# Optimization experiments

Measured on AMD Instinct MI355X. Metric: run time of the kernel, lower is better.

The kernel has to match this reference:

```python
import jax, jax.numpy as jnp
import numpy as np

EMBED_DIM = 1024
NUM_HEADS = 16
HEAD_DIM = EMBED_DIM // NUM_HEADS
L = 1024  # target/source seq len
N = 2     # batch
EPS = 1e-6


def setup_inputs() -> dict:
    key = jax.random.key(0)
    ks = jax.random.split(key, 11)
    s = 0.02
    return {
        "query": jax.random.normal(ks[0], (L, N, EMBED_DIM), jnp.float32),
        "key": jax.random.normal(ks[1], (L, N, EMBED_DIM), jnp.float32),
        "value": jax.random.normal(ks[2], (L, N, EMBED_DIM), jnp.float32),
        "Wq": jax.random.normal(ks[3], (EMBED_DIM, EMBED_DIM), jnp.float32) * s,
        "bq": jnp.zeros((EMBED_DIM,), jnp.float32),
        "Wk": jax.random.normal(ks[4], (EMBED_DIM, EMBED_DIM), jnp.float32) * s,
        "bk": jnp.zeros((EMBED_DIM,), jnp.float32),
        "Wv": jax.random.normal(ks[5], (EMBED_DIM, EMBED_DIM), jnp.float32) * s,
        "bv": jnp.zeros((EMBED_DIM,), jnp.float32),
        "Wo": jax.random.normal(ks[6], (EMBED_DIM, EMBED_DIM), jnp.float32) * s,
        "bo": jnp.zeros((EMBED_DIM,), jnp.float32),
    }


def _feature_map(x):
    # phi(x) = elu(x) + 1 (Katharopoulos et al., 2020)
    return jax.nn.elu(x) + 1.0


def reference(query, key, value, Wq, bq, Wk, bk, Wv, bv, Wo, bo):
    tgt_len, bsz, embed_dim = query.shape
    H, d = NUM_HEADS, HEAD_DIM
    # projections (torch Linear: x @ W.T + b)
    q = query @ Wq.T + bq
    k = key @ Wk.T + bk
    v = value @ Wv.T + bv
    # (L, N, E) -> (N*H, L, d)
    def to_heads(x):
        return x.reshape(-1, bsz * H, d).transpose(1, 0, 2)
    q, k, v = to_heads(q), to_heads(k), to_heads(v)
    q = _feature_map(q)
    k = _feature_map(k)
    # causal linear attention: S_t = cumsum_s<=t k_s v_s^T ; z_t = cumsum k_s
    kv = jnp.cumsum(jnp.einsum('bld,ble->blde', k, v), axis=1)  # (B*H, L, d, d)
    num = jnp.einsum('bld,blde->ble', q, kv)                    # (B*H, L, d)
    z = jnp.cumsum(k, axis=1)                                   # (B*H, L, d)
    denom = jnp.einsum('bld,bld->bl', q, z) + EPS               # (B*H, L)
    attn = num / denom[..., None]
    # (N*H, L, d) -> (L, N, E)
    attn = attn.transpose(1, 0, 2).reshape(tgt_len, bsz, embed_dim)
    return attn @ Wo.T + bo
```

## Files before the change

### kernel.cpp

```cpp
#include <hip/hip_runtime.h>
#include <cmath>


#define EPS 1e-6f

typedef short bf16x8 __attribute__((ext_vector_type(8)));
typedef float f32x4 __attribute__((ext_vector_type(4)));

__device__ __forceinline__ float b2f(ushort u) {
    union { unsigned u32; float f; } x; x.u32 = ((unsigned)u) << 16; return x.f;
}
__device__ __forceinline__ ushort f2b(float f) {
    union { float f; unsigned u; } x; x.f = f;
    unsigned r = (x.u + 0x7fffu + ((x.u >> 16) & 1u)) >> 16;
    return (ushort)r;
}
__device__ __forceinline__ void gload16(const void* g, void* l) {
    __builtin_amdgcn_global_load_lds(
        (__attribute__((address_space(1))) void*)(uintptr_t)g,
        (__attribute__((address_space(3))) void*)l,
        16, 0, 0);
}

template<int KSTEPS>
__device__ __forceinline__ void gemm_mainloop8(const ushort* __restrict__ A,
                                               const ushort* __restrict__ B,
                                               int brow, int bcol, int kbeg,
                                               ushort* Sh, f32x4 acc[4][4]) {
    const int K = 1024;
    const int BUFE = 8192;
    int tid = threadIdx.x;
    int w = tid >> 6, lane = tid & 63;
    int fr = lane & 15, hi = lane >> 4;
    int wr = w >> 1, wc = w & 1;

    const ushort* gsrc[4];
    int ldst[4];
    #pragma unroll
    for (int i = 0; i < 4; i++) {
        int s = (w * 4 + i) * 64 + lane;
        const ushort* base; int r, c;
        if (s < 512) { r = s >> 2; c = s & 3; base = A + (size_t)(brow + r) * K; }
        else { int s2 = s - 512; r = s2 >> 2; c = s2 & 3; base = B + (size_t)(bcol + r) * K; }
        gsrc[i] = base + kbeg + ((c ^ ((r >> 1) & 3)) * 8);
        ldst[i] = (w * 4 + i) * 512;
    }

    int ea[4], eb[4];
    #pragma unroll
    for (int m = 0; m < 4; m++) {
        int ra = wr * 64 + m * 16 + fr;
        ea[m] = ra * 32 + ((hi ^ ((ra >> 1) & 3)) * 8);
    }
    #pragma unroll
    for (int n = 0; n < 4; n++) {
        int rb = wc * 64 + n * 16 + fr;
        eb[n] = 4096 + rb * 32 + ((hi ^ ((rb >> 1) & 3)) * 8);
    }

    #pragma unroll
    for (int m = 0; m < 4; m++)
        #pragma unroll
        for (int n = 0; n < 4; n++)
            acc[m][n] = (f32x4){0.f, 0.f, 0.f, 0.f};

    #pragma unroll
    for (int i = 0; i < 4; i++) gload16(gsrc[i], Sh + ldst[i]);
    __syncthreads();

    for (int t = 0; t < KSTEPS; ++t) {
        if (t + 1 < KSTEPS) {
            ushort* Sn = Sh + ((t + 1) & 1) * BUFE;
            #pragma unroll
            for (int i = 0; i < 4; i++) gload16(gsrc[i] + (t + 1) * 32, Sn + ldst[i]);
        }
        const ushort* Bc = Sh + (t & 1) * BUFE;
        bf16x8 af[4], bf[4];
        #pragma unroll
        for (int m = 0; m < 4; m++) af[m] = *(const bf16x8*)&Bc[ea[m]];
        #pragma unroll
        for (int n = 0; n < 4; n++) bf[n] = *(const bf16x8*)&Bc[eb[n]];
        #pragma unroll
        for (int m = 0; m < 4; m++)
            #pragma unroll
            for (int n = 0; n < 4; n++)
                acc[m][n] = __builtin_amdgcn_mfma_f32_16x16x32_bf16(af[m], bf[n], acc[m][n], 0, 0, 0);
        __syncthreads();
    }
}

__global__ __launch_bounds__(256) void gemm_proj(
    const ushort* __restrict__ Aq, const ushort* __restrict__ Ak, const ushort* __restrict__ Av,
    const ushort* __restrict__ Bq, const ushort* __restrict__ Bk, const ushort* __restrict__ Bv,
    ushort* __restrict__ pbuf) {
    __shared__ ushort Sh[2 * 8192];
    int bid = blockIdx.x;
    int swz = (bid & 7) * 96 + (bid >> 3);
    int z = swz >> 8;
    int rem = swz & 255;
    int kh = rem >> 7;
    int rem2 = rem & 127;
    int brow = (rem2 >> 3) * 128, bcol = (rem2 & 7) * 128;
    const ushort* A = (z == 0) ? Aq : (z == 1) ? Ak : Av;
    const ushort* B = (z == 0) ? Bq : (z == 1) ? Bk : Bv;
    f32x4 acc[4][4];
    gemm_mainloop8<16>(A, B, brow, bcol, kh * 512, Sh, acc);
    int tid = threadIdx.x, w = tid >> 6, lane = tid & 63;
    int fr = lane & 15, hi = lane >> 4;
    int wr = w >> 1, wc = w & 1;
    ushort* pp = pbuf + (size_t)(z * 2 + kh) * 2097152;
    #pragma unroll
    for (int m = 0; m < 4; m++)
        #pragma unroll
        for (int n = 0; n < 4; n++)
            #pragma unroll
            for (int r = 0; r < 4; r++) {
                int grow = brow + wr * 64 + m * 16 + hi * 4 + r;
                int gcol = bcol + wc * 64 + n * 16 + fr;
                pp[(size_t)grow * 1024 + gcol] = f2b(acc[m][n][r]);
            }
}

__global__ __launch_bounds__(256) void combine_proj(const ushort* __restrict__ pbuf,
                                                    const float* __restrict__ bq,
                                                    const float* __restrict__ bk,
                                                    const float* __restrict__ bv,
                                                    ushort* __restrict__ oq,
                                                    ushort* __restrict__ ok,
                                                    ushort* __restrict__ ov) {
    int z = blockIdx.z;
    int idx = blockIdx.x * 256 + threadIdx.x;
    int row = idx >> 7, c0 = (idx & 127) * 8;
    const float* bias = (z == 0) ? bq : (z == 1) ? bk : bv;
    const ushort* p0 = pbuf + (size_t)(z * 2) * 2097152 + (size_t)row * 1024 + c0;
    bf16x8 a = *(const bf16x8*)p0;
    bf16x8 b = *(const bf16x8*)(p0 + 2097152);
    int l = row >> 1, nb = row & 1, h = c0 >> 6, dd0 = c0 & 63;
    float v[8];
    #pragma unroll
    for (int j = 0; j < 8; j++)
        v[j] = b2f((ushort)a[j]) + b2f((ushort)b[j]) + bias[c0 + j];
    if (z < 2) {
        bf16x8 o;
        #pragma unroll
        for (int j = 0; j < 8; j++) {
            float t = (v[j] > 0.f) ? v[j] + 1.f : __expf(v[j]);
            o[j] = (short)f2b(t);
        }
        ushort* out = (z == 0) ? oq : ok;
        *(bf16x8*)&out[(size_t)((nb * 16 + h) * 1024 + l) * 64 + dd0] = o;
    } else {
        #pragma unroll
        for (int j = 0; j < 8; j++)
            ov[(size_t)((nb * 16 + h) * 64 + dd0 + j) * 1024 + l] = f2b(v[j]);
    }
}

__global__ __launch_bounds__(256) void gemm_outk(const ushort* __restrict__ A,
                                                 const ushort* __restrict__ B,
                                                 ushort* __restrict__ pbuf) {
    __shared__ ushort Sh[2 * 8192];
    int bid = blockIdx.x;
    int swz = (bid & 7) * 64 + (bid >> 3);
    int z = swz >> 7;
    int rem = swz & 127;
    int brow = (rem >> 3) * 128, bcol = (rem & 7) * 128;
    f32x4 acc[4][4];
    gemm_mainloop8<8>(A, B, brow, bcol, z * 256, Sh, acc);
    int tid = threadIdx.x, w = tid >> 6, lane = tid & 63;
    int fr = lane & 15, hi = lane >> 4;
    int wr = w >> 1, wc = w & 1;
    ushort* pp = pbuf + (size_t)z * 2097152;
    #pragma unroll
    for (int m = 0; m < 4; m++)
        #pragma unroll
        for (int n = 0; n < 4; n++)
            #pragma unroll
            for (int r = 0; r < 4; r++) {
                int grow = brow + wr * 64 + m * 16 + hi * 4 + r;
                int gcol = bcol + wc * 64 + n * 16 + fr;
                pp[(size_t)grow * 1024 + gcol] = f2b(acc[m][n][r]);
            }
}

__global__ __launch_bounds__(256) void reduce_out(const ushort* __restrict__ pbuf,
                                                  const float* __restrict__ bias,
                                                  float* __restrict__ out) {
    int idx = blockIdx.x * 256 + threadIdx.x;
    int row = idx >> 7, c0 = (idx & 127) * 8;
    const ushort* p = pbuf + (size_t)row * 1024 + c0;
    bf16x8 a = *(const bf16x8*)p;
    bf16x8 b = *(const bf16x8*)(p + 2097152);
    bf16x8 c = *(const bf16x8*)(p + 4194304);
    bf16x8 d = *(const bf16x8*)(p + 6291456);
    float* o = out + (size_t)row * 1024 + c0;
    #pragma unroll
    for (int j = 0; j < 8; j++)
        o[j] = b2f((ushort)a[j]) + b2f((ushort)b[j]) + b2f((ushort)c[j]) +
               b2f((ushort)d[j]) + bias[c0 + j];
}

__global__ __launch_bounds__(256) void cast_all(
    const float* __restrict__ i0, const float* __restrict__ i1, const float* __restrict__ i2,
    const float* __restrict__ i3, const float* __restrict__ i4, const float* __restrict__ i5,
    const float* __restrict__ i6,
    ushort* __restrict__ o0, ushort* __restrict__ o1, ushort* __restrict__ o2,
    ushort* __restrict__ o3, ushort* __restrict__ o4, ushort* __restrict__ o5,
    ushort* __restrict__ o6) {
    int z = blockIdx.z;
    const float* in = (z == 0) ? i0 : (z == 1) ? i1 : (z == 2) ? i2 :
                      (z == 3) ? i3 : (z == 4) ? i4 : (z == 5) ? i5 : i6;
    ushort* out = (z == 0) ? o0 : (z == 1) ? o1 : (z == 2) ? o2 :
                  (z == 3) ? o3 : (z == 4) ? o4 : (z == 5) ? o5 : o6;
    int n4 = (z < 3) ? 524288 : 262144;
    int i = blockIdx.x * 256 + threadIdx.x;
    if (i < n4) {
        float4 f = ((const float4*)in)[i];
        ushort4 o; o.x = f2b(f.x); o.y = f2b(f.y); o.z = f2b(f.z); o.w = f2b(f.w);
        ((ushort4*)out)[i] = o;
    }
}

__global__ __launch_bounds__(256) void chunk_sums(const ushort* __restrict__ kh,
                                                  const ushort* __restrict__ vt,
                                                  float* __restrict__ St,
                                                  float* __restrict__ zc) {
    int c = blockIdx.x, b = blockIdx.y, tid = threadIdx.x;
    __shared__ float Kl[64][64];
    __shared__ float Vl[64][65];
    const ushort* Kg = kh + (size_t)(b * 1024 + c * 64) * 64;
    for (int i = tid; i < 1024; i += 256) {
        ushort4 k4 = ((const ushort4*)Kg)[i];
        ((float4*)Kl)[i] = make_float4(b2f(k4.x), b2f(k4.y), b2f(k4.z), b2f(k4.w));
        int e = i >> 4, s4 = (i & 15) << 2;
        ushort4 v4 = *(const ushort4*)&vt[(size_t)(b * 64 + e) * 1024 + c * 64 + s4];
        Vl[e][s4 + 0] = b2f(v4.x); Vl[e][s4 + 1] = b2f(v4.y);
        Vl[e][s4 + 2] = b2f(v4.z); Vl[e][s4 + 3] = b2f(v4.w);
    }
    __syncthreads();
    int e = tid & 63, d0 = (tid >> 6) * 16;
    float s[16] = {};
    for (int ss = 0; ss < 64; ss++) {
        float ve = Vl[e][ss];
        #pragma unroll
        for (int i = 0; i < 16; i++) s[i] += Kl[ss][d0 + i] * ve;
    }
    float* So = St + (size_t)(b * 16 + c) * 4096 + e * 64 + d0;
    #pragma unroll
    for (int k = 0; k < 4; k++)
        *(float4*)&So[k * 4] = make_float4(s[4*k], s[4*k+1], s[4*k+2], s[4*k+3]);
    if (tid < 64) {
        float z = 0.f;
        for (int ss = 0; ss < 64; ss++) z += Kl[ss][tid];
        zc[(size_t)(b * 16 + c) * 64 + tid] = z;
    }
}

__global__ __launch_bounds__(256) void prefix_chunks(const float* __restrict__ St,
                                                     ushort* __restrict__ Spt,
                                                     float* __restrict__ zc) {
    int b = blockIdx.x, by = blockIdx.y, tid = threadIdx.x;
    int e = by * 16 + (tid >> 4);
    int d0 = (tid & 15) * 4;
    size_t base = (size_t)b * 65536 + (size_t)e * 64 + d0;
    float run[4] = {};
    for (int c = 0; c < 16; c++) {
        float4 v = *(const float4*)&St[base + (size_t)c * 4096];
        ushort4 o;
        o.x = f2b(run[0]); o.y = f2b(run[1]); o.z = f2b(run[2]); o.w = f2b(run[3]);
        *(ushort4*)&Spt[base + (size_t)c * 4096] = o;
        run[0] += v.x; run[1] += v.y; run[2] += v.z; run[3] += v.w;
    }
    if (by == 0 && tid < 64) {
        float rz = 0.f;
        for (int c = 0; c < 16; c++) {
            size_t idx = ((size_t)b * 16 + c) * 64 + tid;
            float t = zc[idx];
            zc[idx] = rz;
            rz += t;
        }
    }
}

__global__ __launch_bounds__(256) void attn_chunk(const ushort* __restrict__ qh,
                                                  const ushort* __restrict__ kh,
                                                  const ushort* __restrict__ vt,
                                                  const ushort* __restrict__ Spt,
                                                  const float* __restrict__ zc,
                                                  ushort* __restrict__ attn) {
    int c = blockIdx.x, b = blockIdx.y, tid = threadIdx.x;
    int w = tid >> 6, lane = tid & 63;
    int fr = lane & 15, hi = lane >> 4;
    __shared__ ushort Q[4096], Kt[4096], VT[4096], SP[4096], P[4096];
    __shared__ float den[64];

    {
        const ushort* bases[4];
        bases[0] = qh + (size_t)(b * 1024 + c * 64) * 64;
        bases[1] = kh + (size_t)(b * 1024 + c * 64) * 64;
        bases[2] = vt;
        bases[3] = Spt + (size_t)(b * 16 + c) * 4096;
        ushort* dsts[4] = {Q, Kt, VT, SP};
        #pragma unroll
        for (int tl = 0; tl < 4; tl++) {
            #pragma unroll
            for (int j = 0; j < 2; j++) {
                int i = w * 64 + lane + 256 * j;
                int row = i >> 3, sl = i & 7;
                int col = (sl ^ (row & 7)) * 8;
                const ushort* src;
                if (tl == 2) src = vt + (size_t)(b * 64 + row) * 1024 + c * 64 + col;
                else         src = bases[tl] + (size_t)row * 64 + col;
                gload16(src, dsts[tl] + w * 512 + 2048 * j);
            }
        }
    }
    __syncthreads();

    int frow = w * 16 + fr;
    int fkey = fr & 7;
    bf16x8 aq[2];
    #pragma unroll
    for (int kk = 0; kk < 2; kk++)
        aq[kk] = *(const bf16x8*)&Q[frow * 64 + ((kk * 4 + hi) ^ fkey) * 8];
    f32x4 pc[4];
    #pragma unroll
    for (int n = 0; n < 4; n++) {
        pc[n] = (f32x4){0.f, 0.f, 0.f, 0.f};
        #pragma unroll
        for (int kk = 0; kk < 2; kk++) {
            bf16x8 bk_ = *(const bf16x8*)&Kt[(n * 16 + fr) * 64 + ((kk * 4 + hi) ^ fkey) * 8];
            pc[n] = __builtin_amdgcn_mfma_f32_16x16x32_bf16(aq[kk], bk_, pc[n], 0, 0, 0);
        }
    }
    float denp[4] = {0.f, 0.f, 0.f, 0.f};
    #pragma unroll
    for (int n = 0; n < 4; n++)
        #pragma unroll
        for (int r = 0; r < 4; r++) {
            int t = w * 16 + hi * 4 + r;
            int s = n * 16 + fr;
            float v = (s <= t) ? pc[n][r] : 0.f;
            denp[r] += v;
            P[t * 64 + (((s >> 3) ^ (t & 7)) * 8) + (s & 7)] = f2b(v);
        }
    #pragma unroll
    for (int r = 0; r < 4; r++) {
        denp[r] += __shfl_xor(denp[r], 1);
        denp[r] += __shfl_xor(denp[r], 2);
        denp[r] += __shfl_xor(denp[r], 4);
        denp[r] += __shfl_xor(denp[r], 8);
    }
    if (fr == 0) {
        #pragma unroll
        for (int r = 0; r < 4; r++) den[w * 16 + hi * 4 + r] = denp[r];
    }
    __syncthreads();

    if (tid < 64) {
        int t = tid;
        const float* zg = zc + (size_t)(b * 16 + c) * 64;
        float a = 0.f;
        for (int d = 0; d < 64; d++)
            a += b2f(Q[t * 64 + (((d >> 3) ^ (t & 7)) * 8) + (d & 7)]) * zg[d];
        den[t] += a;
    }

    bf16x8 ap[2];
    #pragma unroll
    for (int kk = 0; kk < 2; kk++)
        ap[kk] = *(const bf16x8*)&P[frow * 64 + ((kk * 4 + hi) ^ fkey) * 8];
    f32x4 nacc[4];
    #pragma unroll
    for (int n = 0; n < 4; n++) {
        nacc[n] = (f32x4){0.f, 0.f, 0.f, 0.f};
        #pragma unroll
        for (int kk = 0; kk < 2; kk++) {
            bf16x8 bs = *(const bf16x8*)&SP[(n * 16 + fr) * 64 + ((kk * 4 + hi) ^ fkey) * 8];
            nacc[n] = __builtin_amdgcn_mfma_f32_16x16x32_bf16(aq[kk], bs, nacc[n], 0, 0, 0);
        }
        #pragma unroll
        for (int kk = 0; kk < 2; kk++) {
            bf16x8 bv = *(const bf16x8*)&VT[(n * 16 + fr) * 64 + ((kk * 4 + hi) ^ fkey) * 8];
            nacc[n] = __builtin_amdgcn_mfma_f32_16x16x32_bf16(ap[kk], bv, nacc[n], 0, 0, 0);
        }
    }
    __syncthreads();

    int nb = b >> 4, h = b & 15;
    #pragma unroll
    for (int n = 0; n < 4; n++)
        #pragma unroll
        for (int r = 0; r < 4; r++) {
            int t = w * 16 + hi * 4 + r;
            int e = n * 16 + fr;
            int l = c * 64 + t;
            float val = nacc[n][r] / (den[t] + EPS);
            attn[(size_t)(l * 2 + nb) * 1024 + h * 64 + e] = f2b(val);
        }
}

extern "C" void kernel_launch(void* const* d_in, const int* in_sizes, int n_in,
                              void* d_out, int out_size, void* d_ws, size_t ws_size,
                              hipStream_t stream) {
    const float* query = (const float*)d_in[0];
    const float* key_  = (const float*)d_in[1];
    const float* value = (const float*)d_in[2];
    const float* Wq = (const float*)d_in[3];
    const float* bq = (const float*)d_in[4];
    const float* Wk = (const float*)d_in[5];
    const float* bk = (const float*)d_in[6];
    const float* Wv = (const float*)d_in[7];
    const float* bv = (const float*)d_in[8];
    const float* Wo = (const float*)d_in[9];
    const float* bo = (const float*)d_in[10];

    ushort* qbuf = (ushort*)d_ws;
    ushort* kbuf = qbuf + 2097152;
    ushort* vbuf = kbuf + 2097152;
    ushort* wqb  = vbuf + 2097152;
    ushort* wkb  = wqb + 1048576;
    ushort* wvb  = wkb + 1048576;
    ushort* wob  = wvb + 1048576;
    ushort* qh   = wob + 1048576;
    ushort* kh   = qh + 2097152;
    ushort* vt   = kh + 2097152;
    float*  St   = (float*)(vt + 2097152);
    ushort* Spt  = (ushort*)(St + 2097152);
    float*  zc   = (float*)(Spt + 2097152);
    ushort* pbuf = (ushort*)(zc + 32768);
    ushort* attn = qbuf;

    cast_all<<<dim3(2048, 1, 7), 256, 0, stream>>>(query, key_, value, Wq, Wk, Wv, Wo,
                                                   qbuf, kbuf, vbuf, wqb, wkb, wvb, wob);

    gemm_proj<<<768, 256, 0, stream>>>(qbuf, kbuf, vbuf, wqb, wkb, wvb, pbuf);
    combine_proj<<<dim3(1024, 1, 3), 256, 0, stream>>>(pbuf, bq, bk, bv, qh, kh, vt);

    chunk_sums<<<dim3(16, 32), 256, 0, stream>>>(kh, vt, St, zc);
    prefix_chunks<<<dim3(32, 4), 256, 0, stream>>>(St, Spt, zc);
    attn_chunk<<<dim3(16, 32), 256, 0, stream>>>(qh, kh, vt, Spt, zc, attn);

    gemm_outk<<<512, 256, 0, stream>>>(attn, wob, pbuf);
    reduce_out<<<1024, 256, 0, stream>>>(pbuf, bo, (float*)d_out);
}
```

Measured before the change: 91.79 us.

## Fold projection split-K combine into consumers and drop combine_proj kernel

Removes the separate combine_proj kernel. The V projection now runs without split-K, with bias added and the transposed layout written directly from the GEMM epilogue. The Q and K split-K partials are summed, biased and passed through the elu+1 feature map inside chunk_sums and attn_chunk as they load their tiles. This saves a launch and a full read/write pass over the projection buffers. In exchange, K partials are reduced twice, the loads become strided row gathers, and the V GEMM blocks run twice as long, which may leave a tail.

```diff
diff --git a/kernel.cpp b/kernel.cpp
--- a/kernel.cpp
+++ b/kernel.cpp
@@ -92,67 +92,49 @@
 __global__ __launch_bounds__(256) void gemm_proj(
     const ushort* __restrict__ Aq, const ushort* __restrict__ Ak, const ushort* __restrict__ Av,
     const ushort* __restrict__ Bq, const ushort* __restrict__ Bk, const ushort* __restrict__ Bv,
-    ushort* __restrict__ pbuf) {
+    const float* __restrict__ bv,
+    ushort* __restrict__ pq0, ushort* __restrict__ pq1,
+    ushort* __restrict__ pk0, ushort* __restrict__ pk1,
+    ushort* __restrict__ ov) {
     __shared__ ushort Sh[2 * 8192];
     int bid = blockIdx.x;
-    int swz = (bid & 7) * 96 + (bid >> 3);
-    int z = swz >> 8;
-    int rem = swz & 255;
-    int kh = rem >> 7;
-    int rem2 = rem & 127;
-    int brow = (rem2 >> 3) * 128, bcol = (rem2 & 7) * 128;
-    const ushort* A = (z == 0) ? Aq : (z == 1) ? Ak : Av;
-    const ushort* B = (z == 0) ? Bq : (z == 1) ? Bk : Bv;
+    int swz = (bid & 7) * 80 + (bid >> 3);
+    int zone = swz >> 7;
+    int rem = swz & 127;
+    int brow = (rem >> 3) * 128, bcol = (rem & 7) * 128;
+    const ushort* A = (zone < 2) ? Aq : (zone < 4) ? Ak : Av;
+    const ushort* B = (zone < 2) ? Bq : (zone < 4) ? Bk : Bv;
     f32x4 acc[4][4];
-    gemm_mainloop8<16>(A, B, brow, bcol, kh * 512, Sh, acc);
+    if (zone == 4) gemm_mainloop8<32>(A, B, brow, bcol, 0, Sh, acc);
+    else           gemm_mainloop8<16>(A, B, brow, bcol, (zone & 1) * 512, Sh, acc);
     int tid = threadIdx.x, w = tid >> 6, lane = tid & 63;
     int fr = lane & 15, hi = lane >> 4;
     int wr = w >> 1, wc = w & 1;
-    ushort* pp = pbuf + (size_t)(z * 2 + kh) * 2097152;
-    #pragma unroll
-    for (int m = 0; m < 4; m++)
-        #pragma unroll
-        for (int n = 0; n < 4; n++)
-            #pragma unroll
-            for (int r = 0; r < 4; r++) {
-                int grow = brow + wr * 64 + m * 16 + hi * 4 + r;
-                int gcol = bcol + wc * 64 + n * 16 + fr;
-                pp[(size_t)grow * 1024 + gcol] = f2b(acc[m][n][r]);
-            }
-}
-
-__global__ __launch_bounds__(256) void combine_proj(const ushort* __restrict__ pbuf,
-                                                    const float* __restrict__ bq,
-                                                    const float* __restrict__ bk,
-                                                    const float* __restrict__ bv,
-                                                    ushort* __restrict__ oq,
-                                                    ushort* __restrict__ ok,
-                                                    ushort* __restrict__ ov) {
-    int z = blockIdx.z;
-    int idx = blockIdx.x * 256 + threadIdx.x;
-    int row = idx >> 7, c0 = (idx & 127) * 8;
-    const float* bias = (z == 0) ? bq : (z == 1) ? bk : bv;
-    const ushort* p0 = pbuf + (size_t)(z * 2) * 2097152 + (size_t)row * 1024 + c0;
-    bf16x8 a = *(const bf16x8*)p0;
-    bf16x8 b = *(const bf16x8*)(p0 + 2097152);
-    int l = row >> 1, nb = row & 1, h = c0 >> 6, dd0 = c0 & 63;
-    float v[8];
-    #pragma unroll
-    for (int j = 0; j < 8; j++)
-        v[j] = b2f((ushort)a[j]) + b2f((ushort)b[j]) + bias[c0 + j];
-    if (z < 2) {
-        bf16x8 o;
-        #pragma unroll
-        for (int j = 0; j < 8; j++) {
-            float t = (v[j] > 0.f) ? v[j] + 1.f : __expf(v[j]);
-            o[j] = (short)f2b(t);
-        }
-        ushort* out = (z == 0) ? oq : ok;
-        *(bf16x8*)&out[(size_t)((nb * 16 + h) * 1024 + l) * 64 + dd0] = o;
+    if (zone < 4) {
+        ushort* pp = (zone == 0) ? pq0 : (zone == 1) ? pq1 : (zone == 2) ? pk0 : pk1;
+        #pragma unroll
+        for (int m = 0; m < 4; m++)
+            #pragma unroll
+            for (int n = 0; n < 4; n++)
+                #pragma unroll
+                for (int r = 0; r < 4; r++) {
+                    int grow = brow + wr * 64 + m * 16 + hi * 4 + r;
+                    int gcol = bcol + wc * 64 + n * 16 + fr;
+                    pp[(size_t)grow * 1024 + gcol] = f2b(acc[m][n][r]);
+                }
     } else {
         #pragma unroll
-        for (int j = 0; j < 8; j++)
-            ov[(size_t)((nb * 16 + h) * 64 + dd0 + j) * 1024 + l] = f2b(v[j]);
+        for (int m = 0; m < 4; m++)
+            #pragma unroll
+            for (int n = 0; n < 4; n++)
+                #pragma unroll
+                for (int r = 0; r < 4; r++) {
+                    int grow = brow + wr * 64 + m * 16 + hi * 4 + r;
+                    int gcol = bcol + wc * 64 + n * 16 + fr;
+                    float v = acc[m][n][r] + bv[gcol];
+                    int l = grow >> 1, nb2 = grow & 1, h = gcol >> 6, dd = gcol & 63;
+                    ov[(size_t)((nb2 * 16 + h) * 64 + dd) * 1024 + l] = f2b(v);
+                }
     }
 }
 
@@ -221,17 +203,32 @@
     }
 }
 
-__global__ __launch_bounds__(256) void chunk_sums(const ushort* __restrict__ kh,
+__global__ __launch_bounds__(256) void chunk_sums(const ushort* __restrict__ pk0,
+                                                  const ushort* __restrict__ pk1,
+                                                  const float* __restrict__ bk,
                                                   const ushort* __restrict__ vt,
                                                   float* __restrict__ St,
                                                   float* __restrict__ zc) {
     int c = blockIdx.x, b = blockIdx.y, tid = threadIdx.x;
+    int nb = b >> 4, h = b & 15;
     __shared__ float Kl[64][64];
     __shared__ float Vl[64][65];
-    const ushort* Kg = kh + (size_t)(b * 1024 + c * 64) * 64;
     for (int i = tid; i < 1024; i += 256) {
-        ushort4 k4 = ((const ushort4*)Kg)[i];
-        ((float4*)Kl)[i] = make_float4(b2f(k4.x), b2f(k4.y), b2f(k4.z), b2f(k4.w));
+        int l = i >> 4, d4 = (i & 15) << 2;
+        size_t goff = (size_t)((c * 64 + l) * 2 + nb) * 1024 + h * 64 + d4;
+        ushort4 k0 = *(const ushort4*)&pk0[goff];
+        ushort4 k1 = *(const ushort4*)&pk1[goff];
+        float4 bb = *(const float4*)&bk[h * 64 + d4];
+        float4 kv;
+        kv.x = b2f(k0.x) + b2f(k1.x) + bb.x;
+        kv.y = b2f(k0.y) + b2f(k1.y) + bb.y;
+        kv.z = b2f(k0.z) + b2f(k1.z) + bb.z;
+        kv.w = b2f(k0.w) + b2f(k1.w) + bb.w;
+        kv.x = (kv.x > 0.f) ? kv.x + 1.f : __expf(kv.x);
+        kv.y = (kv.y > 0.f) ? kv.y + 1.f : __expf(kv.y);
+        kv.z = (kv.z > 0.f) ? kv.z + 1.f : __expf(kv.z);
+        kv.w = (kv.w > 0.f) ? kv.w + 1.f : __expf(kv.w);
+        ((float4*)Kl)[i] = kv;
         int e = i >> 4, s4 = (i & 15) << 2;
         ushort4 v4 = *(const ushort4*)&vt[(size_t)(b * 64 + e) * 1024 + c * 64 + s4];
         Vl[e][s4 + 0] = b2f(v4.x); Vl[e][s4 + 1] = b2f(v4.y);
@@ -282,8 +279,12 @@
     }
 }
 
-__global__ __launch_bounds__(256) void attn_chunk(const ushort* __restrict__ qh,
-                                                  const ushort* __restrict__ kh,
+__global__ __launch_bounds__(256) void attn_chunk(const ushort* __restrict__ pq0,
+                                                  const ushort* __restrict__ pq1,
+                                                  const ushort* __restrict__ pk0,
+                                                  const ushort* __restrict__ pk1,
+                                                  const float* __restrict__ bq,
+                                                  const float* __restrict__ bk,
                                                   const ushort* __restrict__ vt,
                                                   const ushort* __restrict__ Spt,
                                                   const float* __restrict__ zc,
@@ -291,18 +292,41 @@
     int c = blockIdx.x, b = blockIdx.y, tid = threadIdx.x;
     int w = tid >> 6, lane = tid & 63;
     int fr = lane & 15, hi = lane >> 4;
+    int nb = b >> 4, h = b & 15;
     __shared__ ushort Q[4096], Kt[4096], VT[4096], SP[4096], P[4096];
     __shared__ float den[64];
 
+    #pragma unroll
+    for (int tl = 0; tl < 2; tl++) {
+        const ushort* P0 = (tl == 0) ? pq0 : pk0;
+        const ushort* P1 = (tl == 0) ? pq1 : pk1;
+        const float* bias = (tl == 0) ? bq : bk;
+        ushort* dst = (tl == 0) ? Q : Kt;
+        #pragma unroll
+        for (int j = 0; j < 2; j++) {
+            int i = w * 64 + lane + 256 * j;
+            int row = i >> 3, sl = i & 7;
+            int col = (sl ^ (row & 7)) * 8;
+            size_t goff = (size_t)((c * 64 + row) * 2 + nb) * 1024 + h * 64 + col;
+            bf16x8 x0 = *(const bf16x8*)&P0[goff];
+            bf16x8 x1 = *(const bf16x8*)&P1[goff];
+            float4 b0 = *(const float4*)&bias[h * 64 + col];
+            float4 b1 = *(const float4*)&bias[h * 64 + col + 4];
+            bf16x8 o;
+            #pragma unroll
+            for (int e = 0; e < 8; e++) {
+                float bb = (e < 4) ? (&b0.x)[e] : (&b1.x)[e - 4];
+                float v = b2f((ushort)x0[e]) + b2f((ushort)x1[e]) + bb;
+                v = (v > 0.f) ? v + 1.f : __expf(v);
+                o[e] = (short)f2b(v);
+            }
+            *(bf16x8*)&dst[i * 8] = o;
+        }
+    }
     {
-        const ushort* bases[4];
-        bases[0] = qh + (size_t)(b * 1024 + c * 64) * 64;
-        bases[1] = kh + (size_t)(b * 1024 + c * 64) * 64;
-        bases[2] = vt;
-        bases[3] = Spt + (size_t)(b * 16 + c) * 4096;
-        ushort* dsts[4] = {Q, Kt, VT, SP};
-        #pragma unroll
-        for (int tl = 0; tl < 4; tl++) {
+        const ushort* Sptb = Spt + (size_t)(b * 16 + c) * 4096;
+        #pragma unroll
+        for (int tl = 2; tl < 4; tl++) {
             #pragma unroll
             for (int j = 0; j < 2; j++) {
                 int i = w * 64 + lane + 256 * j;
@@ -310,8 +334,8 @@
                 int col = (sl ^ (row & 7)) * 8;
                 const ushort* src;
                 if (tl == 2) src = vt + (size_t)(b * 64 + row) * 1024 + c * 64 + col;
-                else         src = bases[tl] + (size_t)row * 64 + col;
-                gload16(src, dsts[tl] + w * 512 + 2048 * j);
+                else         src = Sptb + (size_t)row * 64 + col;
+                gload16(src, (tl == 2 ? VT : SP) + w * 512 + 2048 * j);
             }
         }
     }
@@ -387,7 +411,6 @@
     }
     __syncthreads();
 
-    int nb = b >> 4, h = b & 15;
     #pragma unroll
     for (int n = 0; n < 4; n++)
         #pragma unroll
@@ -422,24 +445,27 @@
     ushort* wkb  = wqb + 1048576;
     ushort* wvb  = wkb + 1048576;
     ushort* wob  = wvb + 1048576;
-    ushort* qh   = wob + 1048576;
-    ushort* kh   = qh + 2097152;
-    ushort* vt   = kh + 2097152;
-    float*  St   = (float*)(vt + 2097152);
+    ushort* vt   = wob + 1048576;
+    ushort* pq0  = vt + 2097152;
+    ushort* pq1  = pq0 + 2097152;
+    ushort* pk0  = pq1 + 2097152;
+    ushort* pk1  = pk0 + 2097152;
+    float*  St   = (float*)(pk1 + 2097152);
     ushort* Spt  = (ushort*)(St + 2097152);
     float*  zc   = (float*)(Spt + 2097152);
-    ushort* pbuf = (ushort*)(zc + 32768);
+    ushort* pbuf = pq0;
     ushort* attn = qbuf;
 
     cast_all<<<dim3(2048, 1, 7), 256, 0, stream>>>(query, key_, value, Wq, Wk, Wv, Wo,
                                                    qbuf, kbuf, vbuf, wqb, wkb, wvb, wob);
 
-    gemm_proj<<<768, 256, 0, stream>>>(qbuf, kbuf, vbuf, wqb, wkb, wvb, pbuf);
-    combine_proj<<<dim3(1024, 1, 3), 256, 0, stream>>>(pbuf, bq, bk, bv, qh, kh, vt);
-
-    chunk_sums<<<dim3(16, 32), 256, 0, stream>>>(kh, vt, St, zc);
+    gemm_proj<<<640, 256, 0, stream>>>(qbuf, kbuf, vbuf, wqb, wkb, wvb, bv,
+                                       pq0, pq1, pk0, pk1, vt);
+
+    chunk_sums<<<dim3(16, 32), 256, 0, stream>>>(pk0, pk1, bk, vt, St, zc);
     prefix_chunks<<<dim3(32, 4), 256, 0, stream>>>(St, Spt, zc);
-    attn_chunk<<<dim3(16, 32), 256, 0, stream>>>(qh, kh, vt, Spt, zc, attn);
+    attn_chunk<<<dim3(16, 32), 256, 0, stream>>>(pq0, pq1, pk0, pk1, bq, bk,
+                                                 vt, Spt, zc, attn);
 
     gemm_outk<<<512, 256, 0, stream>>>(attn, wob, pbuf);
     reduce_out<<<1024, 256, 0, stream>>>(pbuf, bo, (float*)d_out);
```

Measured after the change: 104.6 us. 1.14x slower.
